# Kernel optimization log

Hardware: AMD Instinct MI355X
Metric: run time of the kernel (lower is better)

The kernel has to match this reference:

```python
import jax, jax.numpy as jnp
import numpy as np

N_NODES = 50000
N_EDGES = 1600000
NUM_GRAPHS = 512
HID = 128
EDGE_DIM = 64
N_CONV = 4
BN_EPS = 1e-5


def setup_inputs() -> dict:
    key = jax.random.key(0)
    ks = jax.random.split(key, 16)
    x = jax.random.normal(ks[0], (N_NODES, 9), dtype=jnp.float32)
    edge_index = jax.random.randint(ks[1], (2, N_EDGES), 0, N_NODES, dtype=jnp.int64)
    edge_attr = jax.random.normal(ks[2], (N_EDGES, EDGE_DIM), dtype=jnp.float32)
    batch = jnp.sort(jax.random.randint(ks[3], (N_NODES,), 0, NUM_GRAPHS, dtype=jnp.int64))
    s = 0.05
    W_emb = jax.random.normal(ks[4], (9, HID), dtype=jnp.float32) * s
    b_emb = jnp.zeros((HID,), jnp.float32)
    zin = 2 * HID + EDGE_DIM  # 320: cat([x_i, x_j, edge_attr])
    Wf = jax.random.normal(ks[5], (N_CONV, zin, HID), dtype=jnp.float32) * s
    bf = jnp.zeros((N_CONV, HID), jnp.float32)
    Ws = jax.random.normal(ks[6], (N_CONV, zin, HID), dtype=jnp.float32) * s
    bs = jnp.zeros((N_CONV, HID), jnp.float32)
    gamma = jnp.ones((N_CONV, HID), jnp.float32)
    beta = jnp.zeros((N_CONV, HID), jnp.float32)
    W1 = jax.random.normal(ks[7], (HID, HID // 2), dtype=jnp.float32) * s
    b1 = jnp.zeros((HID // 2,), jnp.float32)
    W2 = jax.random.normal(ks[8], (HID // 2, 1), dtype=jnp.float32) * s
    b2 = jnp.zeros((1,), jnp.float32)
    return dict(x=x, edge_index=edge_index, edge_attr=edge_attr, batch=batch,
                W_emb=W_emb, b_emb=b_emb, Wf=Wf, bf=bf, Ws=Ws, bs=bs,
                gamma=gamma, beta=beta, W1=W1, b1=b1, W2=W2, b2=b2)


def _segment_mean(vals, idx, num_segments):
    s = jax.ops.segment_sum(vals, idx, num_segments=num_segments)
    cnt = jax.ops.segment_sum(jnp.ones((vals.shape[0], 1), vals.dtype), idx,
                              num_segments=num_segments)
    return s / jnp.maximum(cnt, 1.0)


def _forward(x, edge_index, edge_attr, batch, W_emb, b_emb, Wf, bf, Ws, bs,
             gamma, beta, W1, b1, W2, b2):
    src, dst = edge_index[0], edge_index[1]  # x_j = x[src], x_i = x[dst]
    h = x @ W_emb + b_emb  # [N, HID]
    for l in range(N_CONV):
        residual = h
        # lin(cat([x_i, x_j, e])) == x_i@W[:H] + x_j@W[H:2H] + e@W[2H:] + b,
        # with node projections done at N granularity before the edge gather.
        f = (h @ Wf[l, :HID])[dst] + (h @ Wf[l, HID:2 * HID])[src] \
            + edge_attr @ Wf[l, 2 * HID:] + bf[l]
        g = (h @ Ws[l, :HID])[dst] + (h @ Ws[l, HID:2 * HID])[src] \
            + edge_attr @ Ws[l, 2 * HID:] + bs[l]
        msg = jax.nn.sigmoid(f) * jax.nn.softplus(g)  # [E, HID]
        aggr = _segment_mean(msg, dst, N_NODES)
        h_conv = aggr + h  # CGConv internal residual
        # BatchNorm1d (training-mode batch stats, biased variance)
        mu = jnp.mean(h_conv, axis=0)
        var = jnp.mean(jnp.square(h_conv - mu), axis=0)
        h_bn = gamma[l] * (h_conv - mu) * jax.lax.rsqrt(var + BN_EPS) + beta[l]
        h = jax.nn.relu(h_bn) + residual  # dropout = identity (eval)
    pooled = _segment_mean(h, batch, NUM_GRAPHS)  # [G, HID]
    out = jax.nn.softplus(pooled @ W1 + b1) @ W2 + b2
    return out.squeeze(-1)  # [G]


def reference(x, edge_index, edge_attr, batch, W_emb, b_emb, Wf, bf, Ws, bs,
              gamma, beta, W1, b1, W2, b2):
    return _forward(x, edge_index, edge_attr, batch, W_emb, b_emb, Wf, bf,
                    Ws, bs, gamma, beta, W1, b1, W2, b2)
```

## Files before the change

kernel.cpp:

```cpp
#include <hip/hip_runtime.h>
#include <math.h>

#define N_NODES 50000
#define N_EDGES 1600000
#define NGRAPH  512
#define HID     128
#define EDIM    64
#define NCONV   4
#define MAXWI   150064

typedef __attribute__((ext_vector_type(8))) short short8;
typedef __attribute__((ext_vector_type(4))) float f32x4;
typedef unsigned int  u32;
typedef unsigned short u16;

#define MFMA16(a, b, c) __builtin_amdgcn_mfma_f32_16x16x32_bf16(a, b, c, 0, 0, 0)

__device__ __forceinline__ float fsig(float x) {
  return __builtin_amdgcn_rcpf(1.f + __expf(-x));
}
__device__ __forceinline__ float fsp(float x) {
  return fmaxf(x, 0.f) + __logf(1.f + __expf(-fabsf(x)));
}
__device__ __forceinline__ u16 f2bf(float x) {
  u32 u = __float_as_uint(x);
  return (u16)((u + 0x7fff + ((u >> 16) & 1)) >> 16);
}
__device__ __forceinline__ u32 f2bf_pack(float lo, float hi) {
  u32 a = __float_as_uint(lo), b = __float_as_uint(hi);
  u32 ra = (a + 0x7fff + ((a >> 16) & 1)) >> 16;
  u32 rb = (b + 0x7fff + ((b >> 16) & 1)) & 0xffff0000u;
  return ra | rb;
}
__device__ __forceinline__ short8 cvt8(float4 a, float4 b) {
  union { short8 s; u32 u[4]; } r;
  r.u[0] = f2bf_pack(a.x, a.y);
  r.u[1] = f2bf_pack(a.z, a.w);
  r.u[2] = f2bf_pack(b.x, b.y);
  r.u[3] = f2bf_pack(b.z, b.w);
  return r.s;
}

__global__ __launch_bounds__(256) void k_embed(const float* __restrict__ x,
                                               const float* __restrict__ Wemb,
                                               const float* __restrict__ bemb,
                                               float* __restrict__ h,
                                               u16* __restrict__ hb, u16* __restrict__ hlo) {
  int i = blockIdx.x * blockDim.x + threadIdx.x;
  if (i >= N_NODES * HID) return;
  int n = i >> 7, c = i & 127;
  const float* xr = x + (size_t)n * 9;
  float acc = bemb[c];
#pragma unroll
  for (int k = 0; k < 9; k++) acc = fmaf(xr[k], Wemb[k * HID + c], acc);
  h[i] = acc;
  u16 hi16 = f2bf(acc);
  hb[i] = hi16;
  hlo[i] = f2bf(acc - __uint_as_float((u32)hi16 << 16));
}

__global__ __launch_bounds__(256) void k_count(const int* __restrict__ ei, int* __restrict__ cnt) {
  int e = blockIdx.x * blockDim.x + threadIdx.x;
  if (e >= N_EDGES) return;
  atomicAdd(&cnt[ei[N_EDGES + e]], 1);
}

__global__ __launch_bounds__(256) void k_scan1(const int* __restrict__ cnt, int* __restrict__ bsum) {
  __shared__ int s[256];
  int i = blockIdx.x * 256 + threadIdx.x;
  s[threadIdx.x] = (i < N_NODES) ? cnt[i] : 0;
  __syncthreads();
  for (int o = 128; o > 0; o >>= 1) {
    if (threadIdx.x < o) s[threadIdx.x] += s[threadIdx.x + o];
    __syncthreads();
  }
  if (threadIdx.x == 0) bsum[blockIdx.x] = s[0];
}

__global__ __launch_bounds__(256) void k_scan2(int* __restrict__ bsum, int nb) {
  __shared__ int s[256];
  int tid = threadIdx.x;
  s[tid] = (tid < nb) ? bsum[tid] : 0;
  __syncthreads();
  for (int o = 1; o < 256; o <<= 1) {
    int t = (tid >= o) ? s[tid - o] : 0;
    __syncthreads();
    s[tid] += t;
    __syncthreads();
  }
  if (tid < nb) bsum[tid] = (tid == 0) ? 0 : s[tid - 1];
}

__global__ __launch_bounds__(256) void k_scan3(const int* __restrict__ cnt, const int* __restrict__ bsum,
                                               int* __restrict__ row_start, float* __restrict__ inv) {
  __shared__ int s[256];
  int i = blockIdx.x * 256 + threadIdx.x;
  int v = (i < N_NODES) ? cnt[i] : 0;
  s[threadIdx.x] = v;
  __syncthreads();
  for (int o = 1; o < 256; o <<= 1) {
    int t = (threadIdx.x >= o) ? s[threadIdx.x - o] : 0;
    __syncthreads();
    s[threadIdx.x] += t;
    __syncthreads();
  }
  if (i < N_NODES) {
    row_start[i + 1] = s[threadIdx.x] + bsum[blockIdx.x];
    inv[i] = 1.0f / (float)max(v, 1);
    if (i == 0) row_start[0] = 0;
  }
}

__global__ __launch_bounds__(256) void k_fill(const int* __restrict__ ei, const int* __restrict__ row_start,
                                              int* __restrict__ cur, int* __restrict__ eids,
                                              int* __restrict__ esrc) {
  int e = blockIdx.x * blockDim.x + threadIdx.x;
  if (e < 64) {
    eids[N_EDGES + e] = 0;
    esrc[N_EDGES + e] = 0;
  }
  if (e >= N_EDGES) return;
  int s = ei[e], d = ei[N_EDGES + e];
  int pos = row_start[d] + atomicAdd(&cur[d], 1);
  eids[pos] = e;
  esrc[pos] = s;
}

__global__ __launch_bounds__(256) void k_tilecnt(const int* __restrict__ row_start,
                                                 int* __restrict__ tcnt) {
  int i = blockIdx.x * 256 + threadIdx.x;
  if (i >= N_NODES) return;
  tcnt[i] = (row_start[i + 1] - row_start[i] + 15) >> 4;
}

__global__ __launch_bounds__(256) void k_scan3w(const int* __restrict__ tcnt,
                                                const int* __restrict__ bsum,
                                                int* __restrict__ tstart) {
  __shared__ int s[256];
  int i = blockIdx.x * 256 + threadIdx.x;
  int v = (i < N_NODES) ? tcnt[i] : 0;
  s[threadIdx.x] = v;
  __syncthreads();
  for (int o = 1; o < 256; o <<= 1) {
    int t = (threadIdx.x >= o) ? s[threadIdx.x - o] : 0;
    __syncthreads();
    s[threadIdx.x] += t;
    __syncthreads();
  }
  if (i < N_NODES) {
    tstart[i] = s[threadIdx.x] - v + bsum[blockIdx.x];
    if (i == N_NODES - 1) tstart[N_NODES] = s[threadIdx.x] + bsum[blockIdx.x];
  }
}

__global__ __launch_bounds__(256) void k_wfill(const int* __restrict__ row_start,
                                               const int* __restrict__ tstart,
                                               int* __restrict__ wnode, int* __restrict__ wbase) {
  int n = blockIdx.x * 256 + threadIdx.x;
  if (n >= N_NODES) return;
  int rs = row_start[n], re = row_start[n + 1];
  int ts = tstart[n];
  int nt = (re - rs + 15) >> 4;
  for (int mt = 0; mt < nt; ++mt) {
    wnode[ts + mt] = n;
    wbase[ts + mt] = rs + mt * 16;
  }
}

__global__ void k_wpad(const int* __restrict__ tstart,
                       int* __restrict__ wnode, int* __restrict__ wbase) {
  int t = threadIdx.x;
  int nwi = tstart[N_NODES];
  wnode[nwi + t] = 0;
  wbase[nwi + t] = 0;
}

__global__ __launch_bounds__(256) void k_gatherA(const float* __restrict__ eattr,
                                                 const int* __restrict__ eids,
                                                 u16* __restrict__ Ae) {
  int t = blockIdx.x * 256 + threadIdx.x;
  if (t >= (N_EDGES + 64) * 8) return;
  int pos = t >> 3, chunk = t & 7;
  short8* dst = (short8*)((char*)Ae + ((size_t)pos << 7) + (chunk << 4));
  if (pos >= N_EDGES) {
    union { short8 s; u32 u[4]; } z; z.u[0] = z.u[1] = z.u[2] = z.u[3] = 0;
    *dst = z.s;
    return;
  }
  int eid = eids[pos];
  const float* src = eattr + ((size_t)eid << 6) + (chunk << 3);
  float4 a = *(const float4*)src;
  float4 b = *(const float4*)(src + 4);
  *dst = cvt8(a, b);
}

__global__ __launch_bounds__(256) void k_prepW(const float* __restrict__ Wf,
                                               const float* __restrict__ Ws,
                                               u16* __restrict__ Whi, u16* __restrict__ Wlo) {
  int t = blockIdx.x * 256 + threadIdx.x;
  if (t >= 65536 * NCONV) return;
  int l = t >> 16, t16 = t & 65535;
  int c = t16 >> 7, k = t16 & 127;
  int q = c >> 7, col = c & 127;
  const float* W = ((q < 2) ? Wf : Ws) + (size_t)l * 320 * HID;
  int row = (q & 1) ? (128 + k) : k;
  float wv = W[row * HID + col];
  u16 hb16 = f2bf(wv);
  float lo = wv - __uint_as_float((u32)hb16 << 16);
  int nt = (c >> 4) & 7, l15 = c & 15;
  int s = k >> 5, lg = (k >> 3) & 3, i = k & 7;
  int idx = l * 65536 + (((q * 8 + nt) * 4 + s) * 64 + (lg * 16 + l15)) * 8 + i;
  Whi[idx] = hb16;
  Wlo[idx] = f2bf(lo);
}

__global__ __launch_bounds__(256) void k_prepB(const float* __restrict__ Wf,
                                               const float* __restrict__ Ws,
                                               u16* __restrict__ Bhi) {
  int t = blockIdx.x * 256 + threadIdx.x;
  if (t >= 16384 * NCONV) return;
  int l = t >> 14, tid = t & 16383;
  int i = tid & 7, lane = (tid >> 3) & 63, s = (tid >> 9) & 1, nt = tid >> 10;
  int k = s * 32 + ((lane >> 4) << 3) + i;
  int col = ((nt & 7) << 4) + (lane & 15);
  const float* W = ((nt < 8) ? Wf : Ws) + (size_t)l * 320 * HID + 256 * HID;
  Bhi[t] = f2bf(W[k * HID + col]);
}

__global__ __launch_bounds__(256) void k_nodeproj_mfma(
    const u16* __restrict__ hb, const u16* __restrict__ hlo,
    const u16* __restrict__ Whi, const u16* __restrict__ Wlo,
    const float* __restrict__ bf_l, const float* __restrict__ bs_l,
    float* __restrict__ Pd, u32* __restrict__ Ppk) {
  const int lane = threadIdx.x & 63, w = threadIdx.x >> 6;
  const int l15 = lane & 15, lg = lane >> 4;
  const int nb = blockIdx.x * 16;
  const short8* WH = (const short8*)Whi;
  const short8* WL = (const short8*)Wlo;
  f32x4 acc[8];
#pragma unroll
  for (int nt = 0; nt < 8; nt++) acc[nt] = (f32x4){0.f, 0.f, 0.f, 0.f};
  const u32 arow = ((u32)(nb + l15)) << 8;
#pragma unroll
  for (int s = 0; s < 4; s++) {
    u32 ao = arow + (s << 6) + (lg << 4);
    short8 ah = *(const short8*)((const char*)hb + ao);
    short8 al = *(const short8*)((const char*)hlo + ao);
#pragma unroll
    for (int nt = 0; nt < 8; nt++) {
      int bi = ((w * 8 + nt) * 4 + s) * 64 + lane;
      short8 bhv = WH[bi];
      short8 blv = WL[bi];
      acc[nt] = MFMA16(ah, bhv, acc[nt]);
      acc[nt] = MFMA16(ah, blv, acc[nt]);
      acc[nt] = MFMA16(al, bhv, acc[nt]);
    }
  }
  if ((w & 1) == 0) {
    const float* bias = (w == 0) ? bf_l : bs_l;
    int pdoff = (w == 0) ? 0 : 128;
#pragma unroll
    for (int nt = 0; nt < 8; nt++) {
      int col = nt * 16 + l15;
      float b = bias[col];
#pragma unroll
      for (int r = 0; r < 4; r++) {
        int node = nb + lg * 4 + r;
        Pd[(size_t)node * 256 + pdoff + col] = acc[nt][r] + b;
      }
    }
  } else {
    int off = (w == 1) ? 0 : 1;
#pragma unroll
    for (int g = 0; g < 4; g++) {
#pragma unroll
      for (int r = 0; r < 4; r++) {
        int node = nb + lg * 4 + r;
        Ppk[(size_t)node * 128 + 2 * (g * 16 + l15) + off] =
            f2bf_pack(acc[2 * g][r], acc[2 * g + 1][r]);
      }
    }
  }
}

__global__ __launch_bounds__(256, 4) void k_edge_wl(
    const float* __restrict__ Pd, const u32* __restrict__ Ppk,
    const u16* __restrict__ Ae, const int* __restrict__ row_start,
    const int* __restrict__ esrc, const u16* __restrict__ Bhi,
    const int* __restrict__ wnode, const int* __restrict__ wbase,
    const int* __restrict__ tstart, float* __restrict__ aggr) {
  const int tid = threadIdx.x;
  const int lane = tid & 63;
  const int w = tid >> 6;
  const int l15 = lane & 15, lg = lane >> 4;
  const int cb = w * 32;

  const int NWI = tstart[N_NODES];
  int C = (NWI + (int)gridDim.x - 1) / (int)gridDim.x;
  int k0 = (int)blockIdx.x * C;
  int k1 = min(k0 + C, NWI);
  if (k0 >= k1) return;

  const short8* BH = (const short8*)Bhi;
  short8 bh[4][2];
  const int nts[4] = {2 * w, 2 * w + 1, 8 + 2 * w, 9 + 2 * w};
#pragma unroll
  for (int t = 0; t < 4; t++) {
#pragma unroll
    for (int s = 0; s < 2; s++) bh[t][s] = BH[(nts[t] * 2 + s) * 64 + lane];
  }

  const u32 poff = ((u32)(w * 16 + l15)) << 3;
  const int eoff = lg << 2;
  const char* aeb = (const char*)Ae;
  const char* ppb = (const char*)Ppk;

  int wn0 = wnode[k0],     wb0 = wbase[k0];
  int wn1 = wnode[k0 + 1], wb1 = wbase[k0 + 1];
  int wn2 = wnode[k0 + 2], wb2 = wbase[k0 + 2];
  int re0 = row_start[wn0 + 1];
  const float* Pn0 = Pd + (size_t)wn0 * 256;
  float fd0 = Pn0[cb + l15], fd1 = Pn0[cb + 16 + l15];
  float gd0 = Pn0[128 + cb + l15], gd1 = Pn0[128 + cb + 16 + l15];
  uint2 gc0, gc1, gc2, gc3;
  {
    const int* ep0 = esrc + wb0 + eoff;
    int a = ep0[0], b = ep0[1], c2 = ep0[2], d = ep0[3];
    gc0 = *(const uint2*)(ppb + (((u32)a) << 9) + poff);
    gc1 = *(const uint2*)(ppb + (((u32)b) << 9) + poff);
    gc2 = *(const uint2*)(ppb + (((u32)c2) << 9) + poff);
    gc3 = *(const uint2*)(ppb + (((u32)d) << 9) + poff);
  }
  const int* ep1 = esrc + wb1 + eoff;
  int sA0 = ep1[0], sA1 = ep1[1], sA2 = ep1[2], sA3 = ep1[3];
  u32 ab = ((u32)(wb0 + l15) << 7) + ((u32)lg << 4);
  short8 ac0 = *(const short8*)(aeb + ab);
  short8 ac1 = *(const short8*)(aeb + ab + 64);

  float acc0 = 0.f, acc1 = 0.f;

  for (int k = k0; k < k1; ++k) {
    uint2 gn0 = *(const uint2*)(ppb + (((u32)sA0) << 9) + poff);
    uint2 gn1 = *(const uint2*)(ppb + (((u32)sA1) << 9) + poff);
    uint2 gn2 = *(const uint2*)(ppb + (((u32)sA2) << 9) + poff);
    uint2 gn3 = *(const uint2*)(ppb + (((u32)sA3) << 9) + poff);
    int wn3 = wnode[k + 3], wb3 = wbase[k + 3];
    const int* ep2 = esrc + wb2 + eoff;
    int t0 = ep2[0], t1 = ep2[1], t2 = ep2[2], t3 = ep2[3];
    int re1 = row_start[wn1 + 1];
    const float* Pn1 = Pd + (size_t)wn1 * 256;
    float nfd0 = Pn1[cb + l15], nfd1 = Pn1[cb + 16 + l15];
    float ngd0 = Pn1[128 + cb + l15], ngd1 = Pn1[128 + cb + 16 + l15];

    f32x4 d0 = {fd0, fd0, fd0, fd0};
    f32x4 d1 = {fd1, fd1, fd1, fd1};
    f32x4 d2 = {gd0, gd0, gd0, gd0};
    f32x4 d3 = {gd1, gd1, gd1, gd1};
    d0 = MFMA16(ac0, bh[0][0], d0); d0 = MFMA16(ac1, bh[0][1], d0);
    d1 = MFMA16(ac0, bh[1][0], d1); d1 = MFMA16(ac1, bh[1][1], d1);
    d2 = MFMA16(ac0, bh[2][0], d2); d2 = MFMA16(ac1, bh[2][1], d2);
    d3 = MFMA16(ac0, bh[3][0], d3); d3 = MFMA16(ac1, bh[3][1], d3);

    u32 ab1 = ((u32)(wb1 + l15) << 7) + ((u32)lg << 4);
    ac0 = *(const short8*)(aeb + ab1);
    ac1 = *(const short8*)(aeb + ab1 + 64);

    const uint2 pgr[4] = {gc0, gc1, gc2, gc3};
    int rowlim = re0 - wb0;
    bool fullt = (rowlim >= 16);
#pragma unroll
    for (int r = 0; r < 4; r++) {
      uint2 pg = pgr[r];
      float f0 = d0[r] + __uint_as_float(pg.x << 16);
      float f1 = d1[r] + __uint_as_float(pg.x & 0xffff0000u);
      float g0 = d2[r] + __uint_as_float(pg.y << 16);
      float g1 = d3[r] + __uint_as_float(pg.y & 0xffff0000u);
      float m0 = fsig(f0) * fsp(g0);
      float m1 = fsig(f1) * fsp(g1);
      if (!fullt) {
        int row = (lg << 2) + r;
        if (row >= rowlim) { m0 = 0.f; m1 = 0.f; }
      }
      acc0 += m0;
      acc1 += m1;
    }

    if (wn0 != wn1 || k == k1 - 1) {
      acc0 += __shfl_xor(acc0, 16); acc0 += __shfl_xor(acc0, 32);
      acc1 += __shfl_xor(acc1, 16); acc1 += __shfl_xor(acc1, 32);
      if (lane < 16) {
        atomicAdd(&aggr[(size_t)wn0 * HID + cb + lane], acc0);
      } else if (lane < 32) {
        atomicAdd(&aggr[(size_t)wn0 * HID + cb + 16 + l15], acc1);
      }
      acc0 = 0.f; acc1 = 0.f;
    }

    wn0 = wn1; wb0 = wb1; wn1 = wn2; wb1 = wb2; wn2 = wn3; wb2 = wb3;
    re0 = re1;
    fd0 = nfd0; fd1 = nfd1; gd0 = ngd0; gd1 = ngd1;
    gc0 = gn0; gc1 = gn1; gc2 = gn2; gc3 = gn3;
    sA0 = t0; sA1 = t1; sA2 = t2; sA3 = t3;
  }
}

__global__ __launch_bounds__(256) void k_stats(float* __restrict__ hconv,
                                               const float* __restrict__ h,
                                               const float* __restrict__ inv,
                                               float* __restrict__ stats) {
  __shared__ float sb[512];
  int c = threadIdx.x & 127;
  float s1 = 0.f, s2 = 0.f;
  for (int i = blockIdx.x * 256 + threadIdx.x; i < N_NODES * HID; i += gridDim.x * 256) {
    float v = hconv[i] * inv[i >> 7] + h[i];
    hconv[i] = v;
    s1 += v;
    s2 += v * v;
  }
  sb[threadIdx.x] = s1;
  sb[256 + threadIdx.x] = s2;
  __syncthreads();
  if (threadIdx.x < 128) {
    atomicAdd(&stats[c], sb[threadIdx.x] + sb[threadIdx.x + 128]);
    atomicAdd(&stats[128 + c], sb[256 + threadIdx.x] + sb[256 + threadIdx.x + 128]);
  }
}

__global__ __launch_bounds__(256) void k_bn3(const float* __restrict__ hconv, float* __restrict__ h,
                                             const float* __restrict__ stats,
                                             const float* __restrict__ gamma,
                                             const float* __restrict__ beta,
                                             u16* __restrict__ hb, u16* __restrict__ hlo) {
  __shared__ float ssl[256];
  int t = threadIdx.x;
  if (t < 128) {
    float mu = stats[t] * (1.f / N_NODES);
    float var = stats[128 + t] * (1.f / N_NODES) - mu * mu;
    float sc = gamma[t] * rsqrtf(var + 1e-5f);
    ssl[t] = sc;
    ssl[128 + t] = beta[t] - mu * sc;
  }
  __syncthreads();
  int i = blockIdx.x * 256 + t;
  if (i >= N_NODES * HID) return;
  int c = i & 127;
  float v = hconv[i] * ssl[c] + ssl[128 + c];
  float hn = fmaxf(v, 0.f) + h[i];
  h[i] = hn;
  u16 hi16 = f2bf(hn);
  hb[i] = hi16;
  hlo[i] = f2bf(hn - __uint_as_float((u32)hi16 << 16));
}

__global__ __launch_bounds__(128) void k_pool(const float* __restrict__ h, const int* __restrict__ batch,
                                              float* __restrict__ pooled) {
  int g = blockIdx.x;
  int c = threadIdx.x;
  int lo = 0, hi = N_NODES;
  while (lo < hi) { int m = (lo + hi) >> 1; if (batch[m] < g) lo = m + 1; else hi = m; }
  int s = lo;
  lo = 0; hi = N_NODES;
  while (lo < hi) { int m = (lo + hi) >> 1; if (batch[m] < g + 1) lo = m + 1; else hi = m; }
  int e = lo;
  float acc = 0.f;
  for (int n = s; n < e; n++) acc += h[(size_t)n * HID + c];
  pooled[(size_t)g * HID + c] = acc / (float)max(e - s, 1);
}

__global__ __launch_bounds__(64) void k_head(const float* __restrict__ pooled, const float* __restrict__ W1,
                                             const float* __restrict__ b1, const float* __restrict__ W2,
                                             const float* __restrict__ b2, float* __restrict__ out) {
  int g = blockIdx.x;
  int j = threadIdx.x;
  float acc = b1[j];
#pragma unroll 16
  for (int k = 0; k < 128; k++) acc = fmaf(pooled[(size_t)g * HID + k], W1[k * 64 + j], acc);
  float z = fmaxf(acc, 0.f) + __logf(1.f + __expf(-fabsf(acc)));
  float v = z * W2[j];
  for (int o = 32; o > 0; o >>= 1) v += __shfl_down(v, o);
  if (j == 0) out[g] = v + b2[0];
}

extern "C" void kernel_launch(void* const* d_in, const int* in_sizes, int n_in,
                              void* d_out, int out_size, void* d_ws, size_t ws_size,
                              hipStream_t stream) {
  const float* x     = (const float*)d_in[0];
  const int*   ei    = (const int*)d_in[1];
  const float* eattr = (const float*)d_in[2];
  const int*   batch = (const int*)d_in[3];
  const float* Wemb  = (const float*)d_in[4];
  const float* bemb  = (const float*)d_in[5];
  const float* Wf    = (const float*)d_in[6];
  const float* bf    = (const float*)d_in[7];
  const float* Ws    = (const float*)d_in[8];
  const float* bs    = (const float*)d_in[9];
  const float* gamma = (const float*)d_in[10];
  const float* beta  = (const float*)d_in[11];
  const float* W1    = (const float*)d_in[12];
  const float* b1    = (const float*)d_in[13];
  const float* W2    = (const float*)d_in[14];
  const float* b2    = (const float*)d_in[15];
  float* out = (float*)d_out;

  char* ws = (char*)d_ws;
  size_t off = 0;
  auto alloc = [&](size_t bytes) -> char* {
    char* p = ws + off;
    off += (bytes + 255) & ~(size_t)255;
    return p;
  };
  float* h         = (float*)alloc((size_t)N_NODES * HID * 4);
  u16*   hb        = (u16*)alloc((size_t)N_NODES * HID * 2);
  u16*   hlo       = (u16*)alloc((size_t)N_NODES * HID * 2);
  float* Pd        = (float*)alloc((size_t)N_NODES * 256 * 4);
  u32*   Ppk       = (u32*)alloc((size_t)N_NODES * 128 * 4);
  float* hconv     = (float*)alloc((size_t)N_NODES * HID * 4);
  int*   row_start = (int*)alloc((size_t)(N_NODES + 1) * 4);
  float* inv       = (float*)alloc((size_t)N_NODES * 4);
  int*   eids      = (int*)alloc((size_t)(N_EDGES + 64) * 4);
  int*   esrc      = (int*)alloc((size_t)(N_EDGES + 64) * 4);
  u16*   Ae        = (u16*)alloc((size_t)(N_EDGES + 64) * EDIM * 2);
  u16*   Bhi       = (u16*)alloc((size_t)16384 * NCONV * 2);
  u16*   Whi       = (u16*)alloc((size_t)65536 * NCONV * 2);
  u16*   Wlo       = (u16*)alloc((size_t)65536 * NCONV * 2);
  int*   tcnt      = (int*)alloc((size_t)N_NODES * 4);
  int*   tstart    = (int*)alloc((size_t)(N_NODES + 1) * 4);
  int*   wnode     = (int*)alloc((size_t)MAXWI * 4);
  int*   wbase     = (int*)alloc((size_t)MAXWI * 4);
  int*   bsum2     = (int*)alloc(256 * 4);
  char*  zbase     = ws + off;
  int*   cnt       = (int*)alloc((size_t)N_NODES * 4);
  int*   cur       = (int*)alloc((size_t)N_NODES * 4);
  float* stats     = (float*)alloc((size_t)NCONV * 256 * 4);
  size_t zbytes    = (size_t)((ws + off) - zbase);
  int*   bsum      = (int*)alloc(256 * 4);
  float* pooled    = (float*)alloc((size_t)NGRAPH * HID * 4);
  (void)ws_size; (void)in_sizes; (void)n_in; (void)out_size;

  hipMemsetAsync(zbase, 0, zbytes, stream);

  k_embed<<<(N_NODES * HID + 255) / 256, 256, 0, stream>>>(x, Wemb, bemb, h, hb, hlo);

  k_count<<<(N_EDGES + 255) / 256, 256, 0, stream>>>(ei, cnt);
  int nb = (N_NODES + 255) / 256;
  k_scan1<<<nb, 256, 0, stream>>>(cnt, bsum);
  k_scan2<<<1, 256, 0, stream>>>(bsum, nb);
  k_scan3<<<nb, 256, 0, stream>>>(cnt, bsum, row_start, inv);
  k_fill<<<(N_EDGES + 255) / 256, 256, 0, stream>>>(ei, row_start, cur, eids, esrc);
  k_gatherA<<<((N_EDGES + 64) * 8 + 255) / 256, 256, 0, stream>>>(eattr, eids, Ae);

  k_tilecnt<<<nb, 256, 0, stream>>>(row_start, tcnt);
  k_scan1<<<nb, 256, 0, stream>>>(tcnt, bsum2);
  k_scan2<<<1, 256, 0, stream>>>(bsum2, nb);
  k_scan3w<<<nb, 256, 0, stream>>>(tcnt, bsum2, tstart);
  k_wfill<<<nb, 256, 0, stream>>>(row_start, tstart, wnode, wbase);
  k_wpad<<<1, 64, 0, stream>>>(tstart, wnode, wbase);

  k_prepW<<<65536 * NCONV / 256, 256, 0, stream>>>(Wf, Ws, Whi, Wlo);
  k_prepB<<<16384 * NCONV / 256, 256, 0, stream>>>(Wf, Ws, Bhi);

  for (int l = 0; l < NCONV; l++) {
    k_nodeproj_mfma<<<N_NODES / 16, 256, 0, stream>>>(hb, hlo, Whi + l * 65536, Wlo + l * 65536,
                                                      bf + l * HID, bs + l * HID, Pd, Ppk);
    hipMemsetAsync(hconv, 0, (size_t)N_NODES * HID * 4, stream);
    k_edge_wl<<<2560, 256, 0, stream>>>(Pd, Ppk, Ae, row_start, esrc,
                                        Bhi + l * 16384, wnode, wbase, tstart, hconv);
    k_stats<<<128, 256, 0, stream>>>(hconv, h, inv, stats + l * 256);
    k_bn3<<<(N_NODES * HID + 255) / 256, 256, 0, stream>>>(hconv, h, stats + l * 256,
                                                           gamma + l * HID, beta + l * HID,
                                                           hb, hlo);
  }

  k_pool<<<NGRAPH, HID, 0, stream>>>(h, batch, pooled);
  k_head<<<NGRAPH, 64, 0, stream>>>(pooled, W1, b1, W2, b2, out);
}
```

Measured before the change: 2.061 ms.

## Process 32 nodes per node-projection block, raise edge occupancy, widen stats grid

The node-projection MFMA kernel now handles two 16-node row tiles per block, so each loaded weight fragment feeds six MFMAs instead of three and half as many blocks are launched. Node buffers are padded to cover the partial last tile. The edge kernel's launch bounds ask for 5 blocks per CU instead of 4, which limits registers per thread and risks spills. The BN statistics kernel launches 2048 blocks instead of 128 to spread the reduction across more CUs.

```diff
diff --git a/kernel.cpp b/kernel.cpp
--- a/kernel.cpp
+++ b/kernel.cpp
@@ -8,6 +8,7 @@
 #define EDIM    64
 #define NCONV   4
 #define MAXWI   150064
+#define NPAD    (N_NODES + 32)
 
 typedef __attribute__((ext_vector_type(8))) short short8;
 typedef __attribute__((ext_vector_type(4))) float f32x4;
@@ -234,56 +235,71 @@
     float* __restrict__ Pd, u32* __restrict__ Ppk) {
   const int lane = threadIdx.x & 63, w = threadIdx.x >> 6;
   const int l15 = lane & 15, lg = lane >> 4;
-  const int nb = blockIdx.x * 16;
+  const int nb = blockIdx.x * 32;
   const short8* WH = (const short8*)Whi;
   const short8* WL = (const short8*)Wlo;
-  f32x4 acc[8];
-#pragma unroll
-  for (int nt = 0; nt < 8; nt++) acc[nt] = (f32x4){0.f, 0.f, 0.f, 0.f};
-  const u32 arow = ((u32)(nb + l15)) << 8;
+  f32x4 acc[2][8];
+#pragma unroll
+  for (int m = 0; m < 2; m++)
+#pragma unroll
+    for (int nt = 0; nt < 8; nt++) acc[m][nt] = (f32x4){0.f, 0.f, 0.f, 0.f};
+  const u32 arow0 = ((u32)(nb + l15)) << 8;
+  const u32 arow1 = ((u32)(nb + 16 + l15)) << 8;
 #pragma unroll
   for (int s = 0; s < 4; s++) {
-    u32 ao = arow + (s << 6) + (lg << 4);
-    short8 ah = *(const short8*)((const char*)hb + ao);
-    short8 al = *(const short8*)((const char*)hlo + ao);
+    u32 ao0 = arow0 + (s << 6) + (lg << 4);
+    u32 ao1 = arow1 + (s << 6) + (lg << 4);
+    short8 ah0 = *(const short8*)((const char*)hb + ao0);
+    short8 al0 = *(const short8*)((const char*)hlo + ao0);
+    short8 ah1 = *(const short8*)((const char*)hb + ao1);
+    short8 al1 = *(const short8*)((const char*)hlo + ao1);
 #pragma unroll
     for (int nt = 0; nt < 8; nt++) {
       int bi = ((w * 8 + nt) * 4 + s) * 64 + lane;
       short8 bhv = WH[bi];
       short8 blv = WL[bi];
-      acc[nt] = MFMA16(ah, bhv, acc[nt]);
-      acc[nt] = MFMA16(ah, blv, acc[nt]);
-      acc[nt] = MFMA16(al, bhv, acc[nt]);
+      acc[0][nt] = MFMA16(ah0, bhv, acc[0][nt]);
+      acc[0][nt] = MFMA16(ah0, blv, acc[0][nt]);
+      acc[0][nt] = MFMA16(al0, bhv, acc[0][nt]);
+      acc[1][nt] = MFMA16(ah1, bhv, acc[1][nt]);
+      acc[1][nt] = MFMA16(ah1, blv, acc[1][nt]);
+      acc[1][nt] = MFMA16(al1, bhv, acc[1][nt]);
     }
   }
   if ((w & 1) == 0) {
     const float* bias = (w == 0) ? bf_l : bs_l;
     int pdoff = (w == 0) ? 0 : 128;
 #pragma unroll
-    for (int nt = 0; nt < 8; nt++) {
-      int col = nt * 16 + l15;
-      float b = bias[col];
-#pragma unroll
-      for (int r = 0; r < 4; r++) {
-        int node = nb + lg * 4 + r;
-        Pd[(size_t)node * 256 + pdoff + col] = acc[nt][r] + b;
+    for (int m = 0; m < 2; m++) {
+#pragma unroll
+      for (int nt = 0; nt < 8; nt++) {
+        int col = nt * 16 + l15;
+        float b = bias[col];
+#pragma unroll
+        for (int r = 0; r < 4; r++) {
+          int node = nb + m * 16 + lg * 4 + r;
+          Pd[(size_t)node * 256 + pdoff + col] = acc[m][nt][r] + b;
+        }
       }
     }
   } else {
     int off = (w == 1) ? 0 : 1;
 #pragma unroll
-    for (int g = 0; g < 4; g++) {
-#pragma unroll
-      for (int r = 0; r < 4; r++) {
-        int node = nb + lg * 4 + r;
-        Ppk[(size_t)node * 128 + 2 * (g * 16 + l15) + off] =
-            f2bf_pack(acc[2 * g][r], acc[2 * g + 1][r]);
+    for (int m = 0; m < 2; m++) {
+#pragma unroll
+      for (int g = 0; g < 4; g++) {
+#pragma unroll
+        for (int r = 0; r < 4; r++) {
+          int node = nb + m * 16 + lg * 4 + r;
+          Ppk[(size_t)node * 128 + 2 * (g * 16 + l15) + off] =
+              f2bf_pack(acc[m][2 * g][r], acc[m][2 * g + 1][r]);
+        }
       }
     }
   }
 }
 
-__global__ __launch_bounds__(256, 4) void k_edge_wl(
+__global__ __launch_bounds__(256, 5) void k_edge_wl(
     const float* __restrict__ Pd, const u32* __restrict__ Ppk,
     const u16* __restrict__ Ae, const int* __restrict__ row_start,
     const int* __restrict__ esrc, const u16* __restrict__ Bhi,
@@ -510,10 +526,10 @@
     return p;
   };
   float* h         = (float*)alloc((size_t)N_NODES * HID * 4);
-  u16*   hb        = (u16*)alloc((size_t)N_NODES * HID * 2);
-  u16*   hlo       = (u16*)alloc((size_t)N_NODES * HID * 2);
-  float* Pd        = (float*)alloc((size_t)N_NODES * 256 * 4);
-  u32*   Ppk       = (u32*)alloc((size_t)N_NODES * 128 * 4);
+  u16*   hb        = (u16*)alloc((size_t)NPAD * HID * 2);
+  u16*   hlo       = (u16*)alloc((size_t)NPAD * HID * 2);
+  float* Pd        = (float*)alloc((size_t)NPAD * 256 * 4);
+  u32*   Ppk       = (u32*)alloc((size_t)NPAD * 128 * 4);
   float* hconv     = (float*)alloc((size_t)N_NODES * HID * 4);
   int*   row_start = (int*)alloc((size_t)(N_NODES + 1) * 4);
   float* inv       = (float*)alloc((size_t)N_NODES * 4);
@@ -560,12 +576,13 @@
   k_prepB<<<16384 * NCONV / 256, 256, 0, stream>>>(Wf, Ws, Bhi);
 
   for (int l = 0; l < NCONV; l++) {
-    k_nodeproj_mfma<<<N_NODES / 16, 256, 0, stream>>>(hb, hlo, Whi + l * 65536, Wlo + l * 65536,
+    k_nodeproj_mfma<<<(N_NODES + 31) / 32, 256, 0, stream>>>(hb, hlo,
+                                                      Whi + l * 65536, Wlo + l * 65536,
                                                       bf + l * HID, bs + l * HID, Pd, Ppk);
     hipMemsetAsync(hconv, 0, (size_t)N_NODES * HID * 4, stream);
     k_edge_wl<<<2560, 256, 0, stream>>>(Pd, Ppk, Ae, row_start, esrc,
                                         Bhi + l * 16384, wnode, wbase, tstart, hconv);
-    k_stats<<<128, 256, 0, stream>>>(hconv, h, inv, stats + l * 256);
+    k_stats<<<2048, 256, 0, stream>>>(hconv, h, inv, stats + l * 256);
     k_bn3<<<(N_NODES * HID + 255) / 256, 256, 0, stream>>>(hconv, h, stats + l * 256,
                                                            gamma + l * HID, beta + l * HID,
                                                            hb, hlo);
```

Result: faster. 1.902 ms (-7.7%).
